# Performance work log

Measured on AMD Instinct MI355X. Metric: run time of the kernel, lower is better.

The kernel has to match this reference:

```python
import jax, jax.numpy as jnp
import numpy as np
from jax import lax

DIM = 256
HEADS = 8
DIM_HEAD = 64
INNER = HEADS * DIM_HEAD  # 512
K = 3
PAD = K // 2
KV_STRIDE = 2
SCALE = DIM_HEAD ** -0.5
BN_EPS = 1e-5


def _dw_block(x, w_dw, g, b, m, v, w_pw, stride):
    """depthwise conv -> batchnorm (eval) -> 1x1 conv. x: [B,C,H,W]."""
    c = x.shape[1]
    h = lax.conv_general_dilated(
        x, w_dw, window_strides=(stride, stride),
        padding=[(PAD, PAD), (PAD, PAD)],
        feature_group_count=c,
        dimension_numbers=('NCHW', 'OIHW', 'NCHW'))
    inv = lax.rsqrt(v + BN_EPS)
    h = (h - m[None, :, None, None]) * (g * inv)[None, :, None, None] + b[None, :, None, None]
    return jnp.einsum('oc,bchw->bohw', w_pw, h)


def _heads_flat(t):
    # [B, h*d, H, W] -> [B, h, d, H*W]
    B, hd, H, W = t.shape
    return t.reshape(B, HEADS, DIM_HEAD, H * W)


def _cross_attn(q, k, v, Hq, Wq):
    # q: [B,h,d,i], k/v: [B,h,d,j]
    dots = jnp.einsum('bhdi,bhdj->bhij', q, k) * SCALE
    attn = jax.nn.softmax(dots, axis=-1)
    out = jnp.einsum('bhij,bhdj->bhdi', attn, v)
    B = q.shape[0]
    return out.reshape(B, INNER, Hq, Wq)


def _forward(x, y, q_dw_w, q_bn_gamma, q_bn_beta, q_bn_mean, q_bn_var, q_pw_w,
             kv_dw_w, kv_bn_gamma, kv_bn_beta, kv_bn_mean, kv_bn_var, kv_pw_w,
             out_w, out_b):
    B, _, Hx, Wx = x.shape
    _, _, Hy, Wy = y.shape

    qx = _heads_flat(_dw_block(x, q_dw_w, q_bn_gamma, q_bn_beta, q_bn_mean, q_bn_var, q_pw_w, 1))
    kvx = _dw_block(x, kv_dw_w, kv_bn_gamma, kv_bn_beta, kv_bn_mean, kv_bn_var, kv_pw_w, KV_STRIDE)
    kx, vx = map(_heads_flat, jnp.split(kvx, 2, axis=1))

    qy = _heads_flat(_dw_block(y, q_dw_w, q_bn_gamma, q_bn_beta, q_bn_mean, q_bn_var, q_pw_w, 1))
    kvy = _dw_block(y, kv_dw_w, kv_bn_gamma, kv_bn_beta, kv_bn_mean, kv_bn_var, kv_pw_w, KV_STRIDE)
    ky, vy = map(_heads_flat, jnp.split(kvy, 2, axis=1))

    outx = _cross_attn(qx, ky, vy, Hx, Wx)   # x queries attend to y keys/values
    outy = _cross_attn(qy, kx, vx, Hy, Wy)   # y queries attend to x keys/values

    def proj(o):
        return jnp.einsum('oc,bchw->bohw', out_w, o) + out_b[None, :, None, None]

    return proj(outx), proj(outy)


def setup_inputs() -> dict:
    key = jax.random.key(0)
    ks = jax.random.split(key, 8)
    B, H, W = 8, 32, 32
    return {
        'x': jax.random.normal(ks[0], (B, DIM, H, W), jnp.float32),
        'y': jax.random.normal(ks[1], (B, DIM, H, W), jnp.float32),
        'q_dw_w': jax.random.normal(ks[2], (DIM, 1, K, K), jnp.float32) * 0.1,
        'q_bn_gamma': jnp.ones((DIM,), jnp.float32),
        'q_bn_beta': jnp.zeros((DIM,), jnp.float32),
        'q_bn_mean': jnp.zeros((DIM,), jnp.float32),
        'q_bn_var': jnp.ones((DIM,), jnp.float32),
        'q_pw_w': jax.random.normal(ks[3], (INNER, DIM), jnp.float32) * (DIM ** -0.5),
        'kv_dw_w': jax.random.normal(ks[4], (DIM, 1, K, K), jnp.float32) * 0.1,
        'kv_bn_gamma': jnp.ones((DIM,), jnp.float32),
        'kv_bn_beta': jnp.zeros((DIM,), jnp.float32),
        'kv_bn_mean': jnp.zeros((DIM,), jnp.float32),
        'kv_bn_var': jnp.ones((DIM,), jnp.float32),
        'kv_pw_w': jax.random.normal(ks[5], (2 * INNER, DIM), jnp.float32) * (DIM ** -0.5),
        'out_w': jax.random.normal(ks[6], (DIM, INNER), jnp.float32) * (INNER ** -0.5),
        'out_b': jnp.zeros((DIM,), jnp.float32),
    }


def reference(x, y, q_dw_w, q_bn_gamma, q_bn_beta, q_bn_mean, q_bn_var, q_pw_w,
              kv_dw_w, kv_bn_gamma, kv_bn_beta, kv_bn_mean, kv_bn_var, kv_pw_w,
              out_w, out_b):
    return _forward(x, y, q_dw_w, q_bn_gamma, q_bn_beta, q_bn_mean, q_bn_var, q_pw_w,
                    kv_dw_w, kv_bn_gamma, kv_bn_beta, kv_bn_mean, kv_bn_var, kv_pw_w,
                    out_w, out_b)
```

## Files before the change

kernel.cpp:

```cpp
#include <hip/hip_runtime.h>

#define BN_EPS 1e-5f
#define ATT_SCALE 0.125f

typedef _Float16 half_t;
typedef _Float16 half8 __attribute__((ext_vector_type(8)));
typedef _Float16 half4 __attribute__((ext_vector_type(4)));
typedef float f32x4 __attribute__((ext_vector_type(4)));

__device__ __forceinline__ void gll16(const void* g, void* l) {
    __builtin_amdgcn_global_load_lds((const __attribute__((address_space(1))) void*)g,
                                     (__attribute__((address_space(3))) void*)l, 16, 0, 0);
}

__device__ void prep_body(
    int o, int c,
    const float* qg, const float* qb, const float* qm, const float* qv, const float* qpw,
    const float* kg, const float* kbt, const float* km, const float* kvv, const float* kvpw,
    const float* outw,
    half_t* wq, half_t* wkv, half_t* wout, float* bq, float* bkv, float* red)
{
    if (o >= 1536) {
        int ro = o - 1536;
        #pragma unroll
        for (int ci = 0; ci < 2; ++ci) {
            int cc = ci * 256 + c;
            float wv = outw[(size_t)ro * 512 + cc];
            half_t hh = (half_t)wv;
            wout[(size_t)ro * 1024 + cc]       = hh;
            wout[(size_t)ro * 1024 + 512 + cc] = (half_t)(wv - (float)hh);
        }
        return;
    }
    const float *g, *b, *m, *v, *w; half_t* we; float* be;
    if (o < 512) {
        g = qg; b = qb; m = qm; v = qv;
        w = qpw + (size_t)o * 256; we = wq + (size_t)o * 512; be = bq + o;
    } else {
        int ro = o - 512;
        g = kg; b = kbt; m = km; v = kvv;
        w = kvpw + (size_t)ro * 256; we = wkv + (size_t)ro * 512; be = bkv + ro;
    }
    float s  = g[c] * rsqrtf(v[c] + BN_EPS);
    float tt = b[c] - m[c] * s;
    float wv = w[c];
    float wsv = wv * s;
    half_t hh = (half_t)wsv;
    we[c]       = hh;
    we[256 + c] = (half_t)(wsv - (float)hh);
    float partial = wv * tt;
    #pragma unroll
    for (int off = 32; off > 0; off >>= 1)
        partial += __shfl_down(partial, off, 64);
    if ((c & 63) == 0) red[c >> 6] = partial;
    __syncthreads();
    if (c == 0) *be = red[0] + red[1] + red[2] + red[3];
}

__device__ void dw_body(
    int rp, int img, float* sin,
    const float* x, const float* y,
    const float* qdw, const float* kvdw,
    half_t* qB, half_t* kvB)
{
    const float* in = (img < 8) ? x + (size_t)img * 256 * 1024
                                : y + (size_t)(img - 8) * 256 * 1024;
    int t = threadIdx.x;
    int ch = t & 63, cg = t >> 6;
    int r0 = 2 * rp - 1;
    #pragma unroll
    for (int u = t; u < 1024; u += 256) {
        int c = u >> 4, row = (u >> 2) & 3, pi = u & 3;
        sin[c * 148 + row * 36 + (pi < 2 ? pi : 32 + pi)] = 0.f;
    }
    for (int cc = 0; cc < 4; ++cc) {
        __syncthreads();
        #pragma unroll
        for (int ii = 0; ii < 8; ++ii) {
            int u = ii * 256 + t;
            int sch = u >> 5, row = (u >> 3) & 3, seg = u & 7;
            int gr = r0 + row;
            float4 v4 = {0.f, 0.f, 0.f, 0.f};
            if (gr >= 0 && gr < 32)
                v4 = *(const float4*)(in + (size_t)(cc * 64 + sch) * 1024 + gr * 32 + seg * 4);
            float* d = &sin[sch * 148 + row * 36 + 2 + seg * 4];
            d[0] = v4.x; d[1] = v4.y; d[2] = v4.z; d[3] = v4.w;
        }
        __syncthreads();
        int gch = cc * 64 + ch;
        float wq9[9], wk9[9];
        #pragma unroll
        for (int i = 0; i < 9; ++i) { wq9[i] = qdw[gch * 9 + i]; wk9[i] = kvdw[gch * 9 + i]; }
        float rowv[4][12];
        const float* base = &sin[ch * 148];
        #pragma unroll
        for (int rr = 0; rr < 4; ++rr) {
            *(float4*)&rowv[rr][0] = *(const float4*)(base + rr * 36 + cg * 8);
            *(float4*)&rowv[rr][4] = *(const float4*)(base + rr * 36 + cg * 8 + 4);
            *(float4*)&rowv[rr][8] = *(const float4*)(base + rr * 36 + cg * 8 + 8);
        }
        #pragma unroll
        for (int r = 0; r < 2; ++r) {
            #pragma unroll
            for (int c8 = 0; c8 < 8; ++c8) {
                float acc = 0.f;
                #pragma unroll
                for (int dr = 0; dr < 3; ++dr)
                    #pragma unroll
                    for (int dc = 0; dc < 3; ++dc)
                        acc += wq9[dr * 3 + dc] * rowv[r + dr][c8 + dc + 1];
                half_t hh = (half_t)acc;
                size_t p = (size_t)img * 1024 + (2 * rp + r) * 32 + cg * 8 + c8;
                qB[p * 512 + gch]       = hh;
                qB[p * 512 + 256 + gch] = (half_t)(acc - (float)hh);
            }
        }
        #pragma unroll
        for (int c4 = 0; c4 < 4; ++c4) {
            float acc = 0.f;
            #pragma unroll
            for (int dr = 0; dr < 3; ++dr)
                #pragma unroll
                for (int dc = 0; dc < 3; ++dc)
                    acc += wk9[dr * 3 + dc] * rowv[dr][2 * c4 + dc + 1];
            half_t hh = (half_t)acc;
            size_t p = (size_t)img * 256 + rp * 16 + cg * 4 + c4;
            kvB[p * 512 + gch]       = hh;
            kvB[p * 512 + 256 + gch] = (half_t)(acc - (float)hh);
        }
    }
}

__global__ __launch_bounds__(256) void prep_dw_kernel(
    const float* __restrict__ x, const float* __restrict__ y,
    const float* __restrict__ qdw, const float* __restrict__ kvdw,
    const float* __restrict__ qg, const float* __restrict__ qb,
    const float* __restrict__ qm, const float* __restrict__ qv,
    const float* __restrict__ qpw,
    const float* __restrict__ kg, const float* __restrict__ kbt,
    const float* __restrict__ km, const float* __restrict__ kvv,
    const float* __restrict__ kvpw,
    const float* __restrict__ outw,
    half_t* __restrict__ wq, half_t* __restrict__ wkv, half_t* __restrict__ wout,
    float* __restrict__ bq, float* __restrict__ bkv,
    half_t* __restrict__ qB, half_t* __restrict__ kvB)
{
    __shared__ __align__(16) float smem[64 * 148];
    int bx = blockIdx.x;
    if (bx < 256)
        dw_body(bx & 15, bx >> 4, smem, x, y, qdw, kvdw, qB, kvB);
    else
        prep_body(bx - 256, threadIdx.x, qg, qb, qm, qv, qpw,
                  kg, kbt, km, kvv, kvpw, outw, wq, wkv, wout, bq, bkv, smem);
}

template<int MT, int NT, int WGM, int WGN, int NTHR, int MODE>
__device__ __forceinline__ void gemm_worker(
    char* lds, const half_t* Ab, const half_t* Bb,
    void* outBuf, const float* bias,
    int K, int NPX, int img, int m0, int n0, float scale)
{
    constexpr int TM = WGM * MT * 16, TN = WGN * NT * 16;
    constexpr int BUF = (TM + TN) * 128;
    int t = threadIdx.x, w = t >> 6, lane = t & 63, quad = lane >> 4, l15 = lane & 15;
    int wm = w % WGM, wn = w / WGM;
    f32x4 acc[MT][NT] = {};
    const int NC = K / 32;

    auto stage = [&](int kh, int p) {
        char* Ah = lds + p * BUF;
        char* Al = Ah + TM * 64;
        char* Bh = Ah + TM * 128;
        char* Bl = Bh + TN * 64;
        #pragma unroll
        for (int ii = 0; ii < TM * 4 / NTHR; ++ii) {
            int u = ii * NTHR + t;
            int mt = u >> 6, q = (u >> 4) & 3, r = u & 15;
            const half_t* g = Ab + (size_t)(mt * 16 + r) * (2 * K) + kh + q * 8;
            gll16(g,     Ah + (u & ~63) * 16);
            gll16(g + K, Al + (u & ~63) * 16);
        }
        #pragma unroll
        for (int ii = 0; ii < TN * 4 / NTHR; ++ii) {
            int u = ii * NTHR + t;
            int nt = u >> 6, q = (u >> 4) & 3, r = u & 15;
            const half_t* g = Bb + (size_t)(nt * 16 + r) * (2 * K) + kh + q * 8;
            gll16(g,     Bh + (u & ~63) * 16);
            gll16(g + K, Bl + (u & ~63) * 16);
        }
    };

    stage(0, 0);
    for (int kc = 0; kc < NC; ++kc) {
        __syncthreads();
        if (kc + 1 < NC) stage((kc + 1) * 32, (kc + 1) & 1);
        char* Ah = lds + (kc & 1) * BUF;
        char* Al = Ah + TM * 64;
        char* Bh = Ah + TM * 128;
        char* Bl = Bh + TN * 64;
        half8 afh[MT], afl[MT];
        #pragma unroll
        for (int mi = 0; mi < MT; ++mi) {
            afh[mi] = *(half8*)(Ah + (wm * MT + mi) * 1024 + lane * 16);
            afl[mi] = *(half8*)(Al + (wm * MT + mi) * 1024 + lane * 16);
        }
        #pragma unroll
        for (int ni = 0; ni < NT; ++ni) {
            half8 bh = *(half8*)(Bh + (wn * NT + ni) * 1024 + lane * 16);
            half8 bl = *(half8*)(Bl + (wn * NT + ni) * 1024 + lane * 16);
            #pragma unroll
            for (int mi = 0; mi < MT; ++mi) {
                acc[mi][ni] = __builtin_amdgcn_mfma_f32_16x16x32_f16(afh[mi], bh, acc[mi][ni], 0, 0, 0);
                acc[mi][ni] = __builtin_amdgcn_mfma_f32_16x16x32_f16(afh[mi], bl, acc[mi][ni], 0, 0, 0);
                acc[mi][ni] = __builtin_amdgcn_mfma_f32_16x16x32_f16(afl[mi], bh, acc[mi][ni], 0, 0, 0);
            }
        }
    }

    if (MODE == 2) {
        #pragma unroll
        for (int mi = 0; mi < MT; ++mi) {
            int mrow0 = m0 + wm * MT * 16 + mi * 16 + quad * 4;
            #pragma unroll
            for (int ni = 0; ni < NT; ++ni) {
                int col = n0 + wn * NT * 16 + ni * 16 + l15;
                f32x4 a = acc[mi][ni];
                float* op = (float*)outBuf + (size_t)img * 256 * NPX;
                #pragma unroll
                for (int r = 0; r < 4; ++r)
                    op[(size_t)(mrow0 + r) * NPX + col] = a[r] + bias[mrow0 + r];
            }
        }
    } else {
        __syncthreads();
        float* tbuf = (float*)lds;
        constexpr int TP = 40;
        #pragma unroll
        for (int qtr = 0; qtr < TM / 32; ++qtr) {
            #pragma unroll
            for (int mi = 0; mi < MT; ++mi) {
                int rowblk = wm * MT * 16 + mi * 16;
                if (rowblk >= qtr * 32 && rowblk < qtr * 32 + 32) {
                    int mloc = rowblk - qtr * 32 + quad * 4;
                    #pragma unroll
                    for (int ni = 0; ni < NT; ++ni) {
                        int nloc = wn * NT * 16 + ni * 16 + l15;
                        #pragma unroll
                        for (int r = 0; r < 4; ++r) {
                            float vv = acc[mi][ni][r];
                            if (MODE == 0) vv = (vv + bias[m0 + rowblk + quad * 4 + r]) * scale;
                            else           vv = vv + bias[n0 + nloc];
                            tbuf[nloc * TP + mloc + r] = vv;
                        }
                    }
                }
            }
            __syncthreads();
            #pragma unroll
            for (int it = 0; it < (TN * 4) / NTHR; ++it) {
                int u = it * NTHR + t;
                int n = u >> 2, mg = u & 3;
                float vv[8];
                *(float4*)&vv[0] = *(const float4*)&tbuf[n * TP + mg * 8];
                *(float4*)&vv[4] = *(const float4*)&tbuf[n * TP + mg * 8 + 4];
                half8 hv, lv;
                #pragma unroll
                for (int j = 0; j < 8; ++j) {
                    half_t hh = (half_t)vv[j];
                    hv[j] = hh; lv[j] = (half_t)(vv[j] - (float)hh);
                }
                int mglob = m0 + qtr * 32 + mg * 8;
                if (MODE == 0) {
                    int h = mglob >> 6, d0 = mglob & 63;
                    half_t* op = (half_t*)outBuf + ((size_t)(img * 8 + h) * NPX + n0 + n) * 128 + d0;
                    *(half8*)op = hv;
                    *(half8*)(op + 64) = lv;
                } else {
                    int nn = n0 + n, h = nn >> 6, d = nn & 63;
                    half_t* op = (half_t*)outBuf + ((size_t)(img * 8 + h) * 64 + d) * 512 + mglob;
                    *(half8*)op = hv;
                    *(half8*)(op + 256) = lv;
                }
            }
            __syncthreads();
        }
    }
}

__global__ __launch_bounds__(512, 4) void qkv_kernel(
    const half_t* __restrict__ wq, const half_t* __restrict__ wkv,
    const half_t* __restrict__ qB, const half_t* __restrict__ kvB,
    const float* __restrict__ bq, const float* __restrict__ bkv,
    half_t* __restrict__ qpr, half_t* __restrict__ kpr, half_t* __restrict__ vpr)
{
    __shared__ __align__(16) char lds[65536];
    int tile = blockIdx.x, img = blockIdx.z;
    if (tile < 32) {
        int m0 = (tile >> 3) * 128, n0 = (tile & 7) * 128;
        gemm_worker<2, 4, 4, 2, 512, 0>(lds,
            wq + (size_t)m0 * 512,
            qB + (size_t)img * (1024 * 512) + (size_t)n0 * 512,
            qpr, bq, 256, 1024, img, m0, n0, ATT_SCALE);
    } else if (tile < 40) {
        int tt = tile - 32;
        int m0 = (tt >> 1) * 128, n0 = (tt & 1) * 128;
        gemm_worker<2, 4, 4, 2, 512, 0>(lds,
            wkv + (size_t)m0 * 512,
            kvB + (size_t)img * (256 * 512) + (size_t)n0 * 512,
            kpr, bkv, 256, 256, img, m0, n0, 1.0f);
    } else {
        int tt = tile - 40;
        int m0 = (tt >> 2) * 128, n0 = (tt & 3) * 128;
        gemm_worker<2, 4, 4, 2, 512, 1>(lds,
            kvB + (size_t)img * (256 * 512) + (size_t)m0 * 512,
            wkv + (size_t)(512 + n0) * 512,
            vpr, bkv + 512, 256, 512, img, m0, n0, 1.0f);
    }
}

__global__ __launch_bounds__(256, 3) void out_kernel(
    const half_t* __restrict__ wout, const half_t* __restrict__ attp,
    const float* __restrict__ outb, float* __restrict__ out)
{
    __shared__ __align__(16) char lds[49152];
    int tile = blockIdx.x, img = blockIdx.z;
    int m0 = (tile >> 3) * 64, n0 = (tile & 7) * 128;
    gemm_worker<2, 4, 2, 2, 256, 2>(lds,
        wout + (size_t)m0 * 1024,
        attp + (size_t)img * (1024 * 1024) + (size_t)n0 * 1024,
        out, outb, 512, 1024, img, m0, n0, 1.0f);
}

__global__ __launch_bounds__(512, 4) void attn_fused(
    const half_t* __restrict__ qb, const half_t* __restrict__ kb,
    const half_t* __restrict__ vb, half_t* __restrict__ att)
{
    __shared__ __align__(16) char lds[65536];
    int ic = blockIdx.y;
    int img = blockIdx.x & 15, h = blockIdx.x >> 4;
    int partner = img ^ 8;
    int t = threadIdx.x, w = t >> 6, lane = t & 63, quad = lane >> 4, l15 = lane & 15;
    const half_t* qp = qb + ((size_t)(img * 8 + h) * 1024 + ic * 128) * 128;
    const half_t* kp = kb + (size_t)(partner * 8 + h) * 256 * 128;
    const half_t* vp = vb + (size_t)(partner * 8 + h) * 64 * 512;

    half8 qh[2], ql[2];
    #pragma unroll
    for (int kcs = 0; kcs < 2; ++kcs) {
        qh[kcs] = *(const half8*)(qp + (size_t)(w * 16 + l15) * 128 + kcs * 32 + quad * 8);
        ql[kcs] = *(const half8*)(qp + (size_t)(w * 16 + l15) * 128 + 64 + kcs * 32 + quad * 8);
    }

    #pragma unroll
    for (int ii = 0; ii < 4; ++ii) {
        int u = ii * 512 + t;
        const half_t* g = kp + (size_t)((u >> 7) * 16 + (u & 15)) * 128
                             + ((u >> 6) & 1) * 32 + ((u >> 4) & 3) * 8;
        gll16(g,      lds + (u & ~63) * 16);
        gll16(g + 64, lds + 32768 + (u & ~63) * 16);
    }
    __syncthreads();

    f32x4 sacc[16] = {};
    #pragma unroll
    for (int kcs = 0; kcs < 2; ++kcs)
        #pragma unroll
        for (int nt = 0; nt < 16; ++nt) {
            half8 bh = *(const half8*)(lds + (nt * 2 + kcs) * 1024 + lane * 16);
            half8 bl = *(const half8*)(lds + 32768 + (nt * 2 + kcs) * 1024 + lane * 16);
            sacc[nt] = __builtin_amdgcn_mfma_f32_16x16x32_f16(qh[kcs], bh, sacc[nt], 0, 0, 0);
            sacc[nt] = __builtin_amdgcn_mfma_f32_16x16x32_f16(qh[kcs], bl, sacc[nt], 0, 0, 0);
            sacc[nt] = __builtin_amdgcn_mfma_f32_16x16x32_f16(ql[kcs], bh, sacc[nt], 0, 0, 0);
        }

    float mrow[4];
    #pragma unroll
    for (int r = 0; r < 4; ++r) {
        float mx = sacc[0][r];
        #pragma unroll
        for (int nt = 1; nt < 16; ++nt) mx = fmaxf(mx, sacc[nt][r]);
        #pragma unroll
        for (int off = 1; off < 16; off <<= 1) mx = fmaxf(mx, __shfl_xor(mx, off, 64));
        mrow[r] = mx;
    }
    __syncthreads();

    char* Pw = lds + 16384 + w * 4608;
    f32x4 oacc[4] = {};
    float lsum[4] = {0.f, 0.f, 0.f, 0.f};
    for (int jc = 0; jc < 4; ++jc) {
        #pragma unroll
        for (int n4 = 0; n4 < 4; ++n4)
            #pragma unroll
            for (int r = 0; r < 4; ++r) {
                float pv = __expf(sacc[jc * 4 + n4][r] - mrow[r]);
                lsum[r] += pv;
                half_t hh = (half_t)pv;
                int idx = ((quad * 4 + r) * 72 + n4 * 16 + l15) * 2;
                *(half_t*)(Pw + idx) = hh;
                *(half_t*)(Pw + 2304 + idx) = (half_t)(pv - (float)hh);
            }
        __syncthreads();
        {
            const half_t* g = vp + (size_t)(((t >> 7) & 3) * 16 + (t & 15)) * 512
                                 + jc * 64 + ((t >> 6) & 1) * 32 + ((t >> 4) & 3) * 8;
            gll16(g,       lds + (t & ~63) * 16);
            gll16(g + 256, lds + 8192 + (t & ~63) * 16);
        }
        __syncthreads();
        #pragma unroll
        for (int kcs = 0; kcs < 2; ++kcs) {
            half8 ph = *(const half8*)(Pw + (l15 * 72 + kcs * 32 + quad * 8) * 2);
            half8 pl = *(const half8*)(Pw + 2304 + (l15 * 72 + kcs * 32 + quad * 8) * 2);
            #pragma unroll
            for (int nt = 0; nt < 4; ++nt) {
                half8 vh = *(const half8*)(lds + (nt * 2 + kcs) * 1024 + lane * 16);
                half8 vl = *(const half8*)(lds + 8192 + (nt * 2 + kcs) * 1024 + lane * 16);
                oacc[nt] = __builtin_amdgcn_mfma_f32_16x16x32_f16(ph, vh, oacc[nt], 0, 0, 0);
                oacc[nt] = __builtin_amdgcn_mfma_f32_16x16x32_f16(ph, vl, oacc[nt], 0, 0, 0);
                oacc[nt] = __builtin_amdgcn_mfma_f32_16x16x32_f16(pl, vh, oacc[nt], 0, 0, 0);
            }
        }
    }

    float inv[4];
    #pragma unroll
    for (int r = 0; r < 4; ++r) {
        float s = lsum[r];
        #pragma unroll
        for (int off = 1; off < 16; off <<= 1) s += __shfl_xor(s, off, 64);
        inv[r] = 1.f / s;
    }

    __syncthreads();
    #pragma unroll
    for (int nt = 0; nt < 4; ++nt)
        #pragma unroll
        for (int r = 0; r < 4; ++r) {
            float vv = oacc[nt][r] * inv[r];
            half_t hh = (half_t)vv;
            int row = w * 16 + quad * 4 + r, col = nt * 16 + l15;
            *(half_t*)(lds + (row * 132 + col) * 2) = hh;
            *(half_t*)(lds + (row * 132 + 64 + col) * 2) = (half_t)(vv - (float)hh);
        }
    __syncthreads();
    #pragma unroll
    for (int ii = 0; ii < 4; ++ii) {
        int u = ii * 512 + t;
        int i = u >> 4, seg = (u >> 3) & 1, p8 = u & 7;
        half8 val = *(const half8*)(lds + (i * 132 + seg * 64 + p8 * 8) * 2);
        *(half8*)(att + ((size_t)img * 1024 + ic * 128 + i) * 1024 + seg * 512 + h * 64 + p8 * 8) = val;
    }
}

extern "C" void kernel_launch(void* const* d_in, const int* in_sizes, int n_in,
                              void* d_out, int out_size, void* d_ws, size_t ws_size,
                              hipStream_t stream) {
    const float* x    = (const float*)d_in[0];
    const float* y    = (const float*)d_in[1];
    const float* qdw  = (const float*)d_in[2];
    const float* qg   = (const float*)d_in[3];
    const float* qbb  = (const float*)d_in[4];
    const float* qm   = (const float*)d_in[5];
    const float* qv   = (const float*)d_in[6];
    const float* qpw  = (const float*)d_in[7];
    const float* kvdw = (const float*)d_in[8];
    const float* kg   = (const float*)d_in[9];
    const float* kb_  = (const float*)d_in[10];
    const float* km   = (const float*)d_in[11];
    const float* kvv  = (const float*)d_in[12];
    const float* kvpw = (const float*)d_in[13];
    const float* outw = (const float*)d_in[14];
    const float* outb = (const float*)d_in[15];

    char* ws = (char*)d_ws;
    half_t* wq   = (half_t*)(ws);
    half_t* wkv  = (half_t*)(ws + 524288);
    half_t* wout = (half_t*)(ws + 1572864);
    float*  bq   = (float*) (ws + 2097152);
    float*  bkv  = (float*) (ws + 2099200);
    half_t* qpr  = (half_t*)(ws + 2103296);
    half_t* kpr  = (half_t*)(ws + 35657728);
    half_t* vpr  = (half_t*)(ws + 44046336);
    half_t* qB   = (half_t*)(ws + 52434944);
    half_t* kvB  = (half_t*)(ws + 69212160);
    half_t* attp = (half_t*)(ws + 52434944);

    prep_dw_kernel<<<2048, 256, 0, stream>>>(
        x, y, qdw, kvdw, qg, qbb, qm, qv, qpw, kg, kb_, km, kvv, kvpw, outw,
        wq, wkv, wout, bq, bkv, qB, kvB);

    qkv_kernel<<<dim3(48, 1, 16), 512, 0, stream>>>(
        wq, wkv, qB, kvB, bq, bkv, qpr, kpr, vpr);

    attn_fused<<<dim3(128, 8, 1), 512, 0, stream>>>(qpr, kpr, vpr, attp);

    out_kernel<<<dim3(32, 1, 16), 256, 0, stream>>>(wout, attp, outb, (float*)d_out);
}
```

Baseline: 209.8 us.

## Restructure attention kernel to 4 waves with double-buffered K/V streaming

The attention kernel moves from 8 waves of 16 query rows each to 4 waves of 32 query rows each, so every B fragment loaded from LDS feeds twice as many MFMAs. K and V are streamed in chunks through a double-buffered 16KB LDS region instead of loading all of K at once, which cuts LDS use to 32KB so more blocks fit per CU. P tiles and the output staging use XOR swizzles to avoid bank conflicts, and s_setprio is raised around MFMA sections. The costs are higher register pressure from doubled accumulators and more barriers per chunk.

```diff
diff --git a/kernel.cpp b/kernel.cpp
--- a/kernel.cpp
+++ b/kernel.cpp
@@ -331,11 +331,11 @@
         out, outb, 512, 1024, img, m0, n0, 1.0f);
 }
 
-__global__ __launch_bounds__(512, 4) void attn_fused(
+__global__ __launch_bounds__(256, 4) void attn_fused(
     const half_t* __restrict__ qb, const half_t* __restrict__ kb,
     const half_t* __restrict__ vb, half_t* __restrict__ att)
 {
-    __shared__ __align__(16) char lds[65536];
+    __shared__ __align__(16) char lds[32768];
     int ic = blockIdx.y;
     int img = blockIdx.x & 15, h = blockIdx.x >> 4;
     int partner = img ^ 8;
@@ -344,112 +344,159 @@
     const half_t* kp = kb + (size_t)(partner * 8 + h) * 256 * 128;
     const half_t* vp = vb + (size_t)(partner * 8 + h) * 64 * 512;
 
-    half8 qh[2], ql[2];
-    #pragma unroll
-    for (int kcs = 0; kcs < 2; ++kcs) {
-        qh[kcs] = *(const half8*)(qp + (size_t)(w * 16 + l15) * 128 + kcs * 32 + quad * 8);
-        ql[kcs] = *(const half8*)(qp + (size_t)(w * 16 + l15) * 128 + 64 + kcs * 32 + quad * 8);
-    }
-
-    #pragma unroll
-    for (int ii = 0; ii < 4; ++ii) {
-        int u = ii * 512 + t;
-        const half_t* g = kp + (size_t)((u >> 7) * 16 + (u & 15)) * 128
-                             + ((u >> 6) & 1) * 32 + ((u >> 4) & 3) * 8;
-        gll16(g,      lds + (u & ~63) * 16);
-        gll16(g + 64, lds + 32768 + (u & ~63) * 16);
-    }
-    __syncthreads();
-
-    f32x4 sacc[16] = {};
-    #pragma unroll
-    for (int kcs = 0; kcs < 2; ++kcs)
-        #pragma unroll
-        for (int nt = 0; nt < 16; ++nt) {
-            half8 bh = *(const half8*)(lds + (nt * 2 + kcs) * 1024 + lane * 16);
-            half8 bl = *(const half8*)(lds + 32768 + (nt * 2 + kcs) * 1024 + lane * 16);
-            sacc[nt] = __builtin_amdgcn_mfma_f32_16x16x32_f16(qh[kcs], bh, sacc[nt], 0, 0, 0);
-            sacc[nt] = __builtin_amdgcn_mfma_f32_16x16x32_f16(qh[kcs], bl, sacc[nt], 0, 0, 0);
-            sacc[nt] = __builtin_amdgcn_mfma_f32_16x16x32_f16(ql[kcs], bh, sacc[nt], 0, 0, 0);
-        }
-
-    float mrow[4];
-    #pragma unroll
-    for (int r = 0; r < 4; ++r) {
-        float mx = sacc[0][r];
-        #pragma unroll
-        for (int nt = 1; nt < 16; ++nt) mx = fmaxf(mx, sacc[nt][r]);
-        #pragma unroll
-        for (int off = 1; off < 16; off <<= 1) mx = fmaxf(mx, __shfl_xor(mx, off, 64));
-        mrow[r] = mx;
-    }
-    __syncthreads();
-
-    char* Pw = lds + 16384 + w * 4608;
-    f32x4 oacc[4] = {};
-    float lsum[4] = {0.f, 0.f, 0.f, 0.f};
-    for (int jc = 0; jc < 4; ++jc) {
-        #pragma unroll
-        for (int n4 = 0; n4 < 4; ++n4)
+    half8 qh[2][2], ql[2][2];
+    #pragma unroll
+    for (int g = 0; g < 2; ++g)
+        #pragma unroll
+        for (int kcs = 0; kcs < 2; ++kcs) {
+            const half_t* qr = qp + (size_t)(w * 32 + g * 16 + l15) * 128 + kcs * 32 + quad * 8;
+            qh[g][kcs] = *(const half8*)qr;
+            ql[g][kcs] = *(const half8*)(qr + 64);
+        }
+
+    auto stageK = [&](int c, char* buf) {
+        #pragma unroll
+        for (int s = 0; s < 2; ++s) {
+            int sb = s * 4 + w;
+            int plane = sb >> 2, ntr = (sb >> 1) & 1, kcs = sb & 1;
+            const half_t* gp = kp + (size_t)(c * 32 + ntr * 16 + l15) * 128
+                                  + plane * 64 + kcs * 32 + quad * 8;
+            gll16(gp, buf + sb * 1024);
+        }
+    };
+    auto stageV = [&](int c, char* buf) {
+        #pragma unroll
+        for (int s = 0; s < 2; ++s) {
+            int sb = s * 4 + w;
+            int plane = sb >> 2, ntv = sb & 3;
+            const half_t* gp = vp + (size_t)(ntv * 16 + l15) * 512
+                                  + plane * 256 + c * 32 + quad * 8;
+            gll16(gp, buf + sb * 1024);
+        }
+    };
+
+    f32x4 sacc[2][16] = {};
+    stageK(0, lds);
+    #pragma unroll
+    for (int c = 0; c < 8; ++c) {
+        __syncthreads();
+        char* nb = lds + (((c + 1) & 1) * 8192);
+        if (c < 7) stageK(c + 1, nb); else stageV(0, nb);
+        const char* buf = lds + ((c & 1) * 8192);
+        __builtin_amdgcn_s_setprio(1);
+        #pragma unroll
+        for (int kcs = 0; kcs < 2; ++kcs)
+            #pragma unroll
+            for (int ntr = 0; ntr < 2; ++ntr) {
+                half8 bh = *(const half8*)(buf + (ntr * 2 + kcs) * 1024 + lane * 16);
+                half8 bl = *(const half8*)(buf + 4096 + (ntr * 2 + kcs) * 1024 + lane * 16);
+                #pragma unroll
+                for (int g = 0; g < 2; ++g) {
+                    f32x4 a = sacc[g][c * 2 + ntr];
+                    a = __builtin_amdgcn_mfma_f32_16x16x32_f16(qh[g][kcs], bh, a, 0, 0, 0);
+                    a = __builtin_amdgcn_mfma_f32_16x16x32_f16(qh[g][kcs], bl, a, 0, 0, 0);
+                    a = __builtin_amdgcn_mfma_f32_16x16x32_f16(ql[g][kcs], bh, a, 0, 0, 0);
+                    sacc[g][c * 2 + ntr] = a;
+                }
+            }
+        __builtin_amdgcn_s_setprio(0);
+    }
+
+    float mrow[2][4];
+    #pragma unroll
+    for (int g = 0; g < 2; ++g)
+        #pragma unroll
+        for (int r = 0; r < 4; ++r) {
+            float mx = sacc[g][0][r];
+            #pragma unroll
+            for (int nt = 1; nt < 16; ++nt) mx = fmaxf(mx, sacc[g][nt][r]);
+            #pragma unroll
+            for (int off = 1; off < 16; off <<= 1) mx = fmaxf(mx, __shfl_xor(mx, off, 64));
+            mrow[g][r] = mx;
+        }
+
+    char* Pw = lds + 16384 + w * 4096;
+    f32x4 oacc[2][4] = {};
+    float lsum[2][4] = {};
+    #pragma unroll
+    for (int c = 0; c < 8; ++c) {
+        #pragma unroll
+        for (int g = 0; g < 2; ++g)
+            #pragma unroll
+            for (int ntr = 0; ntr < 2; ++ntr)
+                #pragma unroll
+                for (int r = 0; r < 4; ++r) {
+                    float pv = __expf(sacc[g][c * 2 + ntr][r] - mrow[g][r]);
+                    lsum[g][r] += pv;
+                    half_t hh = (half_t)pv;
+                    int off = (((quad * 4 + r) * 64 + (ntr * 16 + l15) * 2) ^ (quad << 4))
+                              + g * 2048;
+                    *(half_t*)(Pw + off)        = hh;
+                    *(half_t*)(Pw + off + 1024) = (half_t)(pv - (float)hh);
+                }
+        __syncthreads();
+        if (c < 7) stageV(c + 1, lds + (((c + 1) & 1) * 8192));
+        const char* buf = lds + ((c & 1) * 8192);
+        half8 ph[2], pl[2];
+        int roff = (l15 * 64 + quad * 16) ^ (((l15 >> 2) & 3) << 4);
+        #pragma unroll
+        for (int g = 0; g < 2; ++g) {
+            ph[g] = *(const half8*)(Pw + g * 2048 + roff);
+            pl[g] = *(const half8*)(Pw + g * 2048 + 1024 + roff);
+        }
+        __builtin_amdgcn_s_setprio(1);
+        #pragma unroll
+        for (int ntv = 0; ntv < 4; ++ntv) {
+            half8 vh = *(const half8*)(buf + ntv * 1024 + lane * 16);
+            half8 vl = *(const half8*)(buf + 4096 + ntv * 1024 + lane * 16);
+            #pragma unroll
+            for (int g = 0; g < 2; ++g) {
+                f32x4 a = oacc[g][ntv];
+                a = __builtin_amdgcn_mfma_f32_16x16x32_f16(ph[g], vh, a, 0, 0, 0);
+                a = __builtin_amdgcn_mfma_f32_16x16x32_f16(ph[g], vl, a, 0, 0, 0);
+                a = __builtin_amdgcn_mfma_f32_16x16x32_f16(pl[g], vh, a, 0, 0, 0);
+                oacc[g][ntv] = a;
+            }
+        }
+        __builtin_amdgcn_s_setprio(0);
+    }
+
+    float inv[2][4];
+    #pragma unroll
+    for (int g = 0; g < 2; ++g)
+        #pragma unroll
+        for (int r = 0; r < 4; ++r) {
+            float s = lsum[g][r];
+            #pragma unroll
+            for (int off = 1; off < 16; off <<= 1) s += __shfl_xor(s, off, 64);
+            inv[g][r] = 1.f / s;
+        }
+
+    #pragma unroll
+    for (int g = 0; g < 2; ++g) {
+        __syncthreads();
+        #pragma unroll
+        for (int ntv = 0; ntv < 4; ++ntv)
             #pragma unroll
             for (int r = 0; r < 4; ++r) {
-                float pv = __expf(sacc[jc * 4 + n4][r] - mrow[r]);
-                lsum[r] += pv;
-                half_t hh = (half_t)pv;
-                int idx = ((quad * 4 + r) * 72 + n4 * 16 + l15) * 2;
-                *(half_t*)(Pw + idx) = hh;
-                *(half_t*)(Pw + 2304 + idx) = (half_t)(pv - (float)hh);
-            }
-        __syncthreads();
-        {
-            const half_t* g = vp + (size_t)(((t >> 7) & 3) * 16 + (t & 15)) * 512
-                                 + jc * 64 + ((t >> 6) & 1) * 32 + ((t >> 4) & 3) * 8;
-            gll16(g,       lds + (t & ~63) * 16);
-            gll16(g + 256, lds + 8192 + (t & ~63) * 16);
-        }
-        __syncthreads();
-        #pragma unroll
-        for (int kcs = 0; kcs < 2; ++kcs) {
-            half8 ph = *(const half8*)(Pw + (l15 * 72 + kcs * 32 + quad * 8) * 2);
-            half8 pl = *(const half8*)(Pw + 2304 + (l15 * 72 + kcs * 32 + quad * 8) * 2);
-            #pragma unroll
-            for (int nt = 0; nt < 4; ++nt) {
-                half8 vh = *(const half8*)(lds + (nt * 2 + kcs) * 1024 + lane * 16);
-                half8 vl = *(const half8*)(lds + 8192 + (nt * 2 + kcs) * 1024 + lane * 16);
-                oacc[nt] = __builtin_amdgcn_mfma_f32_16x16x32_f16(ph, vh, oacc[nt], 0, 0, 0);
-                oacc[nt] = __builtin_amdgcn_mfma_f32_16x16x32_f16(ph, vl, oacc[nt], 0, 0, 0);
-                oacc[nt] = __builtin_amdgcn_mfma_f32_16x16x32_f16(pl, vh, oacc[nt], 0, 0, 0);
-            }
-        }
-    }
-
-    float inv[4];
-    #pragma unroll
-    for (int r = 0; r < 4; ++r) {
-        float s = lsum[r];
-        #pragma unroll
-        for (int off = 1; off < 16; off <<= 1) s += __shfl_xor(s, off, 64);
-        inv[r] = 1.f / s;
-    }
-
-    __syncthreads();
-    #pragma unroll
-    for (int nt = 0; nt < 4; ++nt)
-        #pragma unroll
-        for (int r = 0; r < 4; ++r) {
-            float vv = oacc[nt][r] * inv[r];
-            half_t hh = (half_t)vv;
-            int row = w * 16 + quad * 4 + r, col = nt * 16 + l15;
-            *(half_t*)(lds + (row * 132 + col) * 2) = hh;
-            *(half_t*)(lds + (row * 132 + 64 + col) * 2) = (half_t)(vv - (float)hh);
-        }
-    __syncthreads();
-    #pragma unroll
-    for (int ii = 0; ii < 4; ++ii) {
-        int u = ii * 512 + t;
-        int i = u >> 4, seg = (u >> 3) & 1, p8 = u & 7;
-        half8 val = *(const half8*)(lds + (i * 132 + seg * 64 + p8 * 8) * 2);
-        *(half8*)(att + ((size_t)img * 1024 + ic * 128 + i) * 1024 + seg * 512 + h * 64 + p8 * 8) = val;
+                float vv = oacc[g][ntv][r] * inv[g][r];
+                half_t hh = (half_t)vv;
+                int il = w * 16 + quad * 4 + r;
+                int off = (il * 256 + (ntv * 16 + l15) * 2) ^ (quad << 4);
+                *(half_t*)(lds + off)       = hh;
+                *(half_t*)(lds + off + 128) = (half_t)(vv - (float)hh);
+            }
+        __syncthreads();
+        #pragma unroll
+        for (int ii = 0; ii < 4; ++ii) {
+            int u = ii * 256 + t;
+            int iloc = u >> 4, s16 = u & 15;
+            int off = (iloc * 256 + s16 * 16) ^ (((iloc >> 2) & 3) << 4);
+            half8 val = *(const half8*)(lds + off);
+            int grow = (iloc >> 4) * 32 + g * 16 + (iloc & 15);
+            *(half8*)(att + ((size_t)img * 1024 + ic * 128 + grow) * 1024
+                      + (s16 >> 3) * 512 + h * 64 + (s16 & 7) * 8) = val;
+        }
     }
 }
 
@@ -493,7 +540,7 @@
     qkv_kernel<<<dim3(48, 1, 16), 512, 0, stream>>>(
         wq, wkv, qB, kvB, bq, bkv, qpr, kpr, vpr);
 
-    attn_fused<<<dim3(128, 8, 1), 512, 0, stream>>>(qpr, kpr, vpr, attp);
+    attn_fused<<<dim3(128, 8, 1), 256, 0, stream>>>(qpr, kpr, vpr, attp);
 
     out_kernel<<<dim3(32, 1, 16), 256, 0, stream>>>(wout, attp, outb, (float*)d_out);
 }
```

Measured after the change: 284.2 us. +35.5%, slower.

## Restructure attention into double-buffered K/V streaming with smaller blocks

Applied to the files above, without the earlier changes.

The fused attention kernel now uses 256-thread blocks over 64 query rows, cutting LDS from 64KB to 17KB and doubling the grid. K and V chunks are streamed into double-buffered LDS so loads overlap the MFMA work. The QK product is transposed so probabilities stay in registers as 16x16x16 MFMA operands, which removes the per-wave P staging through LDS. The V layout written by the qkv GEMM is changed to match the new fragment order. The added barriers and setprio hints add scheduling overhead, and the transposed operand layout must still index correctly.

```diff
diff --git a/kernel.cpp b/kernel.cpp
--- a/kernel.cpp
+++ b/kernel.cpp
@@ -277,9 +277,18 @@
                     *(half8*)(op + 64) = lv;
                 } else {
                     int nn = n0 + n, h = nn >> 6, d = nn & 63;
-                    half_t* op = (half_t*)outBuf + ((size_t)(img * 8 + h) * 64 + d) * 512 + mglob;
-                    *(half8*)op = hv;
-                    *(half8*)(op + 256) = lv;
+                    int j0 = mglob;
+                    half_t* op = (half_t*)outBuf + (size_t)(img * 8 + h) * 32768
+                               + (j0 >> 5) * 4096 + ((d >> 4) & 3) * 512 + ((j0 >> 4) & 1) * 256
+                               + ((j0 >> 2) & 3) * 64 + (d & 15) * 4;
+                    half4 a0 = {hv[0], hv[1], hv[2], hv[3]};
+                    half4 a1 = {hv[4], hv[5], hv[6], hv[7]};
+                    half4 b0 = {lv[0], lv[1], lv[2], lv[3]};
+                    half4 b1 = {lv[4], lv[5], lv[6], lv[7]};
+                    *(half4*)op               = a0;
+                    *(half4*)(op + 64)        = a1;
+                    *(half4*)(op + 2048)      = b0;
+                    *(half4*)(op + 2048 + 64) = b1;
                 }
             }
             __syncthreads();
@@ -331,125 +340,139 @@
         out, outb, 512, 1024, img, m0, n0, 1.0f);
 }
 
-__global__ __launch_bounds__(512, 4) void attn_fused(
+__global__ __launch_bounds__(256, 4) void attn_fused(
     const half_t* __restrict__ qb, const half_t* __restrict__ kb,
     const half_t* __restrict__ vb, half_t* __restrict__ att)
 {
-    __shared__ __align__(16) char lds[65536];
-    int ic = blockIdx.y;
+    __shared__ __align__(16) char lds[17408];
+    int ic2 = blockIdx.y;
     int img = blockIdx.x & 15, h = blockIdx.x >> 4;
     int partner = img ^ 8;
     int t = threadIdx.x, w = t >> 6, lane = t & 63, quad = lane >> 4, l15 = lane & 15;
-    const half_t* qp = qb + ((size_t)(img * 8 + h) * 1024 + ic * 128) * 128;
+    const half_t* qp = qb + ((size_t)(img * 8 + h) * 1024 + ic2 * 64) * 128;
     const half_t* kp = kb + (size_t)(partner * 8 + h) * 256 * 128;
-    const half_t* vp = vb + (size_t)(partner * 8 + h) * 64 * 512;
+    const half_t* vp = vb + (size_t)(partner * 8 + h) * 32768;
 
     half8 qh[2], ql[2];
     #pragma unroll
     for (int kcs = 0; kcs < 2; ++kcs) {
-        qh[kcs] = *(const half8*)(qp + (size_t)(w * 16 + l15) * 128 + kcs * 32 + quad * 8);
-        ql[kcs] = *(const half8*)(qp + (size_t)(w * 16 + l15) * 128 + 64 + kcs * 32 + quad * 8);
-    }
-
+        const half_t* qr = qp + (size_t)(w * 16 + l15) * 128 + kcs * 32 + quad * 8;
+        qh[kcs] = *(const half8*)qr;
+        ql[kcs] = *(const half8*)(qr + 64);
+    }
+
+    auto stageK = [&](int c, char* buf) {
+        #pragma unroll
+        for (int s = 0; s < 2; ++s) {
+            int u = s * 256 + t;
+            int sb = u >> 6, li = u & 63;
+            int plane = sb >> 2, ntr = (sb >> 1) & 1, kcs = sb & 1;
+            const half_t* g = kp + (size_t)(c * 32 + ntr * 16 + (li & 15)) * 128
+                                 + plane * 64 + kcs * 32 + (li >> 4) * 8;
+            gll16(g, buf + (u & ~63) * 16);
+        }
+    };
+    auto stageV = [&](int c, char* buf) {
+        #pragma unroll
+        for (int s = 0; s < 2; ++s) {
+            int u = s * 256 + t;
+            gll16(vp + (size_t)c * 4096 + u * 8, buf + (u & ~63) * 16);
+        }
+    };
+
+    f32x4 sacc[16] = {};
+    stageK(0, lds);
+    #pragma unroll
+    for (int c = 0; c < 8; ++c) {
+        __syncthreads();
+        char* nb = lds + (((c + 1) & 1) * 8192);
+        if (c < 7) stageK(c + 1, nb); else stageV(0, nb);
+        const char* buf = lds + ((c & 1) * 8192);
+        __builtin_amdgcn_s_setprio(1);
+        #pragma unroll
+        for (int kcs = 0; kcs < 2; ++kcs)
+            #pragma unroll
+            for (int ntr = 0; ntr < 2; ++ntr) {
+                half8 kh = *(const half8*)(buf + (ntr * 2 + kcs) * 1024 + lane * 16);
+                half8 kl = *(const half8*)(buf + 4096 + (ntr * 2 + kcs) * 1024 + lane * 16);
+                f32x4 s = sacc[c * 2 + ntr];
+                s = __builtin_amdgcn_mfma_f32_16x16x32_f16(kh, qh[kcs], s, 0, 0, 0);
+                s = __builtin_amdgcn_mfma_f32_16x16x32_f16(kh, ql[kcs], s, 0, 0, 0);
+                s = __builtin_amdgcn_mfma_f32_16x16x32_f16(kl, qh[kcs], s, 0, 0, 0);
+                sacc[c * 2 + ntr] = s;
+            }
+        __builtin_amdgcn_s_setprio(0);
+    }
+
+    float mx = sacc[0][0];
+    #pragma unroll
+    for (int ti = 0; ti < 16; ++ti)
+        #pragma unroll
+        for (int r = 0; r < 4; ++r) mx = fmaxf(mx, sacc[ti][r]);
+    mx = fmaxf(mx, __shfl_xor(mx, 16, 64));
+    mx = fmaxf(mx, __shfl_xor(mx, 32, 64));
+
+    f32x4 oacc[4] = {};
+    float lsum = 0.f;
+    #pragma unroll
+    for (int c = 0; c < 8; ++c) {
+        half4 pb[2][2];
+        #pragma unroll
+        for (int kk = 0; kk < 2; ++kk) {
+            f32x4 s = sacc[c * 2 + kk];
+            #pragma unroll
+            for (int e = 0; e < 4; ++e) {
+                float pv = __expf(s[e] - mx);
+                lsum += pv;
+                half_t hh = (half_t)pv;
+                pb[kk][0][e] = hh;
+                pb[kk][1][e] = (half_t)(pv - (float)hh);
+            }
+        }
+        __syncthreads();
+        if (c < 7) stageV(c + 1, lds + (((c + 1) & 1) * 8192));
+        const char* buf = lds + ((c & 1) * 8192);
+        __builtin_amdgcn_s_setprio(1);
+        #pragma unroll
+        for (int mt = 0; mt < 4; ++mt) {
+            #pragma unroll
+            for (int kk = 0; kk < 2; ++kk) {
+                half4 vh = *(const half4*)(buf + (mt * 2 + kk) * 512 + lane * 8);
+                half4 vl = *(const half4*)(buf + 4096 + (mt * 2 + kk) * 512 + lane * 8);
+                f32x4 o = oacc[mt];
+                o = __builtin_amdgcn_mfma_f32_16x16x16f16(vh, pb[kk][0], o, 0, 0, 0);
+                o = __builtin_amdgcn_mfma_f32_16x16x16f16(vh, pb[kk][1], o, 0, 0, 0);
+                o = __builtin_amdgcn_mfma_f32_16x16x16f16(vl, pb[kk][0], o, 0, 0, 0);
+                oacc[mt] = o;
+            }
+        }
+        __builtin_amdgcn_s_setprio(0);
+    }
+
+    lsum += __shfl_xor(lsum, 16, 64);
+    lsum += __shfl_xor(lsum, 32, 64);
+    float inv = 1.f / lsum;
+
+    __syncthreads();
+    #pragma unroll
+    for (int mt = 0; mt < 4; ++mt)
+        #pragma unroll
+        for (int r = 0; r < 4; ++r) {
+            float vv = oacc[mt][r] * inv;
+            half_t hh = (half_t)vv;
+            int row = w * 16 + l15;
+            int d = mt * 16 + quad * 4 + r;
+            *(half_t*)(lds + (row * 132 + d) * 2)      = hh;
+            *(half_t*)(lds + (row * 132 + 64 + d) * 2) = (half_t)(vv - (float)hh);
+        }
+    __syncthreads();
     #pragma unroll
     for (int ii = 0; ii < 4; ++ii) {
-        int u = ii * 512 + t;
-        const half_t* g = kp + (size_t)((u >> 7) * 16 + (u & 15)) * 128
-                             + ((u >> 6) & 1) * 32 + ((u >> 4) & 3) * 8;
-        gll16(g,      lds + (u & ~63) * 16);
-        gll16(g + 64, lds + 32768 + (u & ~63) * 16);
-    }
-    __syncthreads();
-
-    f32x4 sacc[16] = {};
-    #pragma unroll
-    for (int kcs = 0; kcs < 2; ++kcs)
-        #pragma unroll
-        for (int nt = 0; nt < 16; ++nt) {
-            half8 bh = *(const half8*)(lds + (nt * 2 + kcs) * 1024 + lane * 16);
-            half8 bl = *(const half8*)(lds + 32768 + (nt * 2 + kcs) * 1024 + lane * 16);
-            sacc[nt] = __builtin_amdgcn_mfma_f32_16x16x32_f16(qh[kcs], bh, sacc[nt], 0, 0, 0);
-            sacc[nt] = __builtin_amdgcn_mfma_f32_16x16x32_f16(qh[kcs], bl, sacc[nt], 0, 0, 0);
-            sacc[nt] = __builtin_amdgcn_mfma_f32_16x16x32_f16(ql[kcs], bh, sacc[nt], 0, 0, 0);
-        }
-
-    float mrow[4];
-    #pragma unroll
-    for (int r = 0; r < 4; ++r) {
-        float mx = sacc[0][r];
-        #pragma unroll
-        for (int nt = 1; nt < 16; ++nt) mx = fmaxf(mx, sacc[nt][r]);
-        #pragma unroll
-        for (int off = 1; off < 16; off <<= 1) mx = fmaxf(mx, __shfl_xor(mx, off, 64));
-        mrow[r] = mx;
-    }
-    __syncthreads();
-
-    char* Pw = lds + 16384 + w * 4608;
-    f32x4 oacc[4] = {};
-    float lsum[4] = {0.f, 0.f, 0.f, 0.f};
-    for (int jc = 0; jc < 4; ++jc) {
-        #pragma unroll
-        for (int n4 = 0; n4 < 4; ++n4)
-            #pragma unroll
-            for (int r = 0; r < 4; ++r) {
-                float pv = __expf(sacc[jc * 4 + n4][r] - mrow[r]);
-                lsum[r] += pv;
-                half_t hh = (half_t)pv;
-                int idx = ((quad * 4 + r) * 72 + n4 * 16 + l15) * 2;
-                *(half_t*)(Pw + idx) = hh;
-                *(half_t*)(Pw + 2304 + idx) = (half_t)(pv - (float)hh);
-            }
-        __syncthreads();
-        {
-            const half_t* g = vp + (size_t)(((t >> 7) & 3) * 16 + (t & 15)) * 512
-                                 + jc * 64 + ((t >> 6) & 1) * 32 + ((t >> 4) & 3) * 8;
-            gll16(g,       lds + (t & ~63) * 16);
-            gll16(g + 256, lds + 8192 + (t & ~63) * 16);
-        }
-        __syncthreads();
-        #pragma unroll
-        for (int kcs = 0; kcs < 2; ++kcs) {
-            half8 ph = *(const half8*)(Pw + (l15 * 72 + kcs * 32 + quad * 8) * 2);
-            half8 pl = *(const half8*)(Pw + 2304 + (l15 * 72 + kcs * 32 + quad * 8) * 2);
-            #pragma unroll
-            for (int nt = 0; nt < 4; ++nt) {
-                half8 vh = *(const half8*)(lds + (nt * 2 + kcs) * 1024 + lane * 16);
-                half8 vl = *(const half8*)(lds + 8192 + (nt * 2 + kcs) * 1024 + lane * 16);
-                oacc[nt] = __builtin_amdgcn_mfma_f32_16x16x32_f16(ph, vh, oacc[nt], 0, 0, 0);
-                oacc[nt] = __builtin_amdgcn_mfma_f32_16x16x32_f16(ph, vl, oacc[nt], 0, 0, 0);
-                oacc[nt] = __builtin_amdgcn_mfma_f32_16x16x32_f16(pl, vh, oacc[nt], 0, 0, 0);
-            }
-        }
-    }
-
-    float inv[4];
-    #pragma unroll
-    for (int r = 0; r < 4; ++r) {
-        float s = lsum[r];
-        #pragma unroll
-        for (int off = 1; off < 16; off <<= 1) s += __shfl_xor(s, off, 64);
-        inv[r] = 1.f / s;
-    }
-
-    __syncthreads();
-    #pragma unroll
-    for (int nt = 0; nt < 4; ++nt)
-        #pragma unroll
-        for (int r = 0; r < 4; ++r) {
-            float vv = oacc[nt][r] * inv[r];
-            half_t hh = (half_t)vv;
-            int row = w * 16 + quad * 4 + r, col = nt * 16 + l15;
-            *(half_t*)(lds + (row * 132 + col) * 2) = hh;
-            *(half_t*)(lds + (row * 132 + 64 + col) * 2) = (half_t)(vv - (float)hh);
-        }
-    __syncthreads();
-    #pragma unroll
-    for (int ii = 0; ii < 4; ++ii) {
-        int u = ii * 512 + t;
-        int i = u >> 4, seg = (u >> 3) & 1, p8 = u & 7;
-        half8 val = *(const half8*)(lds + (i * 132 + seg * 64 + p8 * 8) * 2);
-        *(half8*)(att + ((size_t)img * 1024 + ic * 128 + i) * 1024 + seg * 512 + h * 64 + p8 * 8) = val;
+        int u = ii * 256 + t;
+        int i = u >> 4, s16 = u & 15;
+        half8 val = *(const half8*)(lds + (i * 132 + (s16 >> 3) * 64 + (s16 & 7) * 8) * 2);
+        *(half8*)(att + ((size_t)img * 1024 + ic2 * 64 + i) * 1024
+                  + (s16 >> 3) * 512 + h * 64 + (s16 & 7) * 8) = val;
     }
 }
 
@@ -493,7 +516,7 @@
     qkv_kernel<<<dim3(48, 1, 16), 512, 0, stream>>>(
         wq, wkv, qB, kvB, bq, bkv, qpr, kpr, vpr);
 
-    attn_fused<<<dim3(128, 8, 1), 512, 0, stream>>>(qpr, kpr, vpr, attp);
+    attn_fused<<<dim3(128, 16, 1), 256, 0, stream>>>(qpr, kpr, vpr, attp);
 
     out_kernel<<<dim3(32, 1, 16), 256, 0, stream>>>(wout, attp, outb, (float*)d_out);
 }
```

New measurement: 213.3 us. About the same (+1.7%).
